# Kernel tuning notes

Hardware: AMD Instinct MI355X
Metric: run time of the kernel (lower is better)

Reference implementation:

```python
import jax, jax.numpy as jnp
import numpy as np

N, E, C, L = 50000, 800000, 64, 3  # nodes, edges, channels, message-passing layers
EPS = 1e-5  # torch.nn.LayerNorm default eps


def _mlp(h, W0, b0, W1, b1, W2, b2, g, beta):
    # MLP(input, hidden=[C, C], output=C) with ReLU between linears, LayerNorm at end
    h = jax.nn.relu(h @ W0 + b0)
    h = jax.nn.relu(h @ W1 + b1)
    h = h @ W2 + b2
    mu = jnp.mean(h, axis=-1, keepdims=True)
    var = jnp.var(h, axis=-1, keepdims=True)
    return (h - mu) * jax.lax.rsqrt(var + EPS) * g + beta


def setup_inputs() -> dict:
    key = jax.random.key(0)
    ks = jax.random.split(key, 12)
    def w(k, shape, fan_in):
        return (jax.random.normal(k, shape, jnp.float32) / np.float32(np.sqrt(fan_in)))
    return {
        "x": jax.random.normal(ks[0], (N, C), jnp.float32),
        "e": jax.random.normal(ks[1], (E, C), jnp.float32),
        "edge_index": jax.random.randint(ks[2], (2, E), 0, N),
        # edge_updater MLP params, stacked over L layers
        "ew0": w(ks[3], (L, 3 * C, C), 3 * C), "eb0": jnp.zeros((L, C), jnp.float32),
        "ew1": w(ks[4], (L, C, C), C),         "eb1": jnp.zeros((L, C), jnp.float32),
        "ew2": w(ks[5], (L, C, C), C),         "eb2": jnp.zeros((L, C), jnp.float32),
        "eg": jnp.ones((L, C), jnp.float32),   "ebt": jnp.zeros((L, C), jnp.float32),
        # node_updater MLP params
        "nw0": w(ks[6], (L, 2 * C, C), 2 * C), "nb0": jnp.zeros((L, C), jnp.float32),
        "nw1": w(ks[7], (L, C, C), C),         "nb1": jnp.zeros((L, C), jnp.float32),
        "nw2": w(ks[8], (L, C, C), C),         "nb2": jnp.zeros((L, C), jnp.float32),
        "ng": jnp.ones((L, C), jnp.float32),   "nbt": jnp.zeros((L, C), jnp.float32),
    }


def reference(x, e, edge_index, ew0, eb0, ew1, eb1, ew2, eb2, eg, ebt,
              nw0, nb0, nw1, nb1, nw2, nb2, ng, nbt):
    src, dst = edge_index[0], edge_index[1]
    for i in range(L):
        # e += edge_updater(cat(x_src, x_dst, e))
        e = e + _mlp(jnp.concatenate([x[src], x[dst], e], axis=1),
                     ew0[i], eb0[i], ew1[i], eb1[i], ew2[i], eb2[i], eg[i], ebt[i])
        # EdgeAggregation(aggr='add'): scatter-add edge features at target nodes
        agg = jax.ops.segment_sum(e, dst, num_segments=N)
        # x += node_updater(cat(x, agg))
        x = x + _mlp(jnp.concatenate([x, agg], axis=1),
                     nw0[i], nb0[i], nw1[i], nb1[i], nw2[i], nb2[i], ng[i], nbt[i])
    return (x, e)
```

## Files before the change

kernel.cpp:

```cpp
#include <hip/hip_runtime.h>

#define CH 64

using bf16x8 = __attribute__((ext_vector_type(8))) short;
using f32x4  = __attribute__((ext_vector_type(4))) float;

__device__ __forceinline__ unsigned short f2bf(float f) {
  unsigned int u = __float_as_uint(f);
  u = (u + 0x7FFFu + ((u >> 16) & 1u)) >> 16;
  return (unsigned short)u;
}

__device__ __forceinline__ bf16x8 pack8(f32x4 a, f32x4 b) {
  bf16x8 r;
  r[0] = (short)f2bf(a[0]); r[1] = (short)f2bf(a[1]);
  r[2] = (short)f2bf(a[2]); r[3] = (short)f2bf(a[3]);
  r[4] = (short)f2bf(b[0]); r[5] = (short)f2bf(b[1]);
  r[6] = (short)f2bf(b[2]); r[7] = (short)f2bf(b[3]);
  return r;
}

#define E0S 200
#define S64 72
#define N0S 136
#define Y68 68

#define EW0_L 0
#define EW1_L 12800
#define EW2_L 17408
#define EW_TOT 22016
#define E_LDS 39424

#define NW0_L 0
#define NW1_L 8704
#define NW2_L 13312
#define NW_TOT 17920
#define N_LDS 26624

#define WS_NW 66048
#define WS_AGG_B    262144
#define WS_ROWPTR_B 13062144
#define WS_NEXT_B   13262208
#define WS_EID_B    13462208

__global__ void prep_w(const float* __restrict__ ew0, const float* __restrict__ ew1,
                       const float* __restrict__ ew2, const float* __restrict__ nw0,
                       const float* __restrict__ nw1, const float* __restrict__ nw2,
                       unsigned short* __restrict__ ws) {
  int i = blockIdx.x * 256 + threadIdx.x;
  if (i < 36864) {
    int l = i / 12288, r = i % 12288, k = r / 64, n = r % 64;
    ws[l * EW_TOT + EW0_L + n * E0S + k] = f2bf(ew0[i]);
  } else if (i < 49152) {
    int j = i - 36864, l = j / 4096, r = j % 4096, k = r / 64, n = r % 64;
    ws[l * EW_TOT + EW1_L + n * S64 + k] = f2bf(ew1[j]);
  } else if (i < 61440) {
    int j = i - 49152, l = j / 4096, r = j % 4096, k = r / 64, n = r % 64;
    ws[l * EW_TOT + EW2_L + n * S64 + k] = f2bf(ew2[j]);
  } else if (i < 86016) {
    int j = i - 61440, l = j / 8192, r = j % 8192, k = r / 64, n = r % 64;
    ws[WS_NW + l * NW_TOT + NW0_L + n * N0S + k] = f2bf(nw0[j]);
  } else if (i < 98304) {
    int j = i - 86016, l = j / 4096, r = j % 4096, k = r / 64, n = r % 64;
    ws[WS_NW + l * NW_TOT + NW1_L + n * S64 + k] = f2bf(nw1[j]);
  } else if (i < 110592) {
    int j = i - 98304, l = j / 4096, r = j % 4096, k = r / 64, n = r % 64;
    ws[WS_NW + l * NW_TOT + NW2_L + n * S64 + k] = f2bf(nw2[j]);
  }
}

__global__ void hist_k(const int* __restrict__ dst, int* __restrict__ counts, int nE) {
  int i = blockIdx.x * 256 + threadIdx.x;
  if (i < nE) atomicAdd(counts + dst[i], 1);
}

__global__ void scan_k(const int* __restrict__ counts, int* __restrict__ row_ptr,
                       int* __restrict__ next, int n) {
  __shared__ int wsum[16];
  __shared__ int chunk_tot;
  __shared__ int base_sh;
  const int tid = threadIdx.x, lane = tid & 63, wv = tid >> 6;
  if (tid == 0) { base_sh = 0; row_ptr[0] = 0; }
  __syncthreads();
  for (int start = 0; start < n; start += 4096) {
    int idx = start + tid * 4;
    int v[4], s = 0;
#pragma unroll
    for (int k = 0; k < 4; ++k) { v[k] = (idx + k < n) ? counts[idx + k] : 0; s += v[k]; }
    int incl = s;
#pragma unroll
    for (int off = 1; off < 64; off <<= 1) {
      int t = __shfl_up(incl, off, 64);
      if (lane >= off) incl += t;
    }
    if (lane == 63) wsum[wv] = incl;
    __syncthreads();
    if (wv == 0 && lane < 16) {
      int w = wsum[lane];
      int wincl = w;
#pragma unroll
      for (int off = 1; off < 16; off <<= 1) {
        int t = __shfl_up(wincl, off, 16);
        if (lane >= off) wincl += t;
      }
      if (lane == 15) chunk_tot = wincl;
      wsum[lane] = wincl - w;
    }
    __syncthreads();
    int run = base_sh + wsum[wv] + (incl - s);
#pragma unroll
    for (int k = 0; k < 4; ++k) {
      int i = idx + k;
      if (i < n) { next[i] = run; run += v[k]; row_ptr[i + 1] = run; }
    }
    __syncthreads();
    if (tid == 0) base_sh += chunk_tot;
    __syncthreads();
  }
}

__global__ void scatter_k(const int* __restrict__ dst, int* __restrict__ next,
                          int* __restrict__ eid, int nE) {
  int i = blockIdx.x * 256 + threadIdx.x;
  if (i < nE) {
    int p = atomicAdd(next + dst[i], 1);
    eid[p] = i;
  }
}

__global__ __launch_bounds__(512, 4)
void edge_kernel(const float* __restrict__ x, const float* e_in, float* e_out,
                 const int* __restrict__ src, const int* __restrict__ dst,
                 const unsigned short* __restrict__ wg,
                 const float* __restrict__ b0, const float* __restrict__ b1,
                 const float* __restrict__ b2, const float* __restrict__ gam,
                 const float* __restrict__ bet, int nE) {
  __shared__ unsigned short lds[E_LDS];
  const int tid = threadIdx.x;
  {
    const uint4* s4 = (const uint4*)wg;
    uint4* d4 = (uint4*)lds;
    for (int i = tid; i < EW_TOT / 8; i += 512) d4[i] = s4[i];
  }
  __syncthreads();

  const int wave = tid >> 6, lane = tid & 63;
  const int quad = lane >> 4, l15 = lane & 15;
  const int EHo = EW_TOT + wave * 2176;
  float* yb = (float*)(lds + EHo);

  float b0c[4], b1c[4], b2c[4], gc[4], btc[4];
#pragma unroll
  for (int j = 0; j < 4; ++j) {
    int col = j * 16 + l15;
    b0c[j] = b0[col]; b1c[j] = b1[col]; b2c[j] = b2[col];
    gc[j] = gam[col]; btc[j] = bet[col];
  }

  const int o1 = quad * 8, o2 = 32 + quad * 8;
  const int gstride = gridDim.x * 128;

  int row0 = blockIdx.x * 128 + wave * 16 + l15;
  int si = src[row0], di = dst[row0];

  for (int base = blockIdx.x * 128; base < nE; base += gstride) {
    const int row = base + wave * 16 + l15;
    const float* er = e_in + (size_t)row * CH;
    f32x4 ve0 = *(const f32x4*)(er + o1);
    f32x4 ve1 = *(const f32x4*)(er + o1 + 4);
    f32x4 ve2 = *(const f32x4*)(er + o2);
    f32x4 ve3 = *(const f32x4*)(er + o2 + 4);
    const float* xs = x + (size_t)si * CH;
    const float* xd = x + (size_t)di * CH;
    bf16x8 af[6];
    {
      f32x4 a0 = *(const f32x4*)(xs + o1);
      f32x4 a1 = *(const f32x4*)(xs + o1 + 4);
      f32x4 a2 = *(const f32x4*)(xs + o2);
      f32x4 a3 = *(const f32x4*)(xs + o2 + 4);
      af[0] = pack8(a0, a1); af[1] = pack8(a2, a3);
    }
    {
      f32x4 a0 = *(const f32x4*)(xd + o1);
      f32x4 a1 = *(const f32x4*)(xd + o1 + 4);
      f32x4 a2 = *(const f32x4*)(xd + o2);
      f32x4 a3 = *(const f32x4*)(xd + o2 + 4);
      af[2] = pack8(a0, a1); af[3] = pack8(a2, a3);
    }
    af[4] = pack8(ve0, ve1); af[5] = pack8(ve2, ve3);

    {
      int nbase = base + gstride;
      if (nbase < nE) {
        int nrow = nbase + wave * 16 + l15;
        si = src[nrow]; di = dst[nrow];
      }
    }

    f32x4 acc0[4];
#pragma unroll
    for (int j = 0; j < 4; ++j) acc0[j] = (f32x4){0.f, 0.f, 0.f, 0.f};
#pragma unroll
    for (int t = 0; t < 6; ++t) {
#pragma unroll
      for (int j = 0; j < 4; ++j) {
        bf16x8 b = *(const bf16x8*)(lds + EW0_L + (j * 16 + l15) * E0S + t * 32 + quad * 8);
        acc0[j] = __builtin_amdgcn_mfma_f32_16x16x32_bf16(af[t], b, acc0[j], 0, 0, 0);
      }
    }
#pragma unroll
    for (int j = 0; j < 4; ++j) {
      int col = j * 16 + l15;
#pragma unroll
      for (int r = 0; r < 4; ++r) {
        float v = fmaxf(acc0[j][r] + b0c[j], 0.f);
        lds[EHo + (quad * 4 + r) * S64 + col] = f2bf(v);
      }
    }
    f32x4 acc1[4];
#pragma unroll
    for (int j = 0; j < 4; ++j) acc1[j] = (f32x4){0.f, 0.f, 0.f, 0.f};
#pragma unroll
    for (int t = 0; t < 2; ++t) {
      bf16x8 a = *(const bf16x8*)(lds + EHo + l15 * S64 + t * 32 + quad * 8);
#pragma unroll
      for (int j = 0; j < 4; ++j) {
        bf16x8 b = *(const bf16x8*)(lds + EW1_L + (j * 16 + l15) * S64 + t * 32 + quad * 8);
        acc1[j] = __builtin_amdgcn_mfma_f32_16x16x32_bf16(a, b, acc1[j], 0, 0, 0);
      }
    }
#pragma unroll
    for (int j = 0; j < 4; ++j) {
      int col = j * 16 + l15;
#pragma unroll
      for (int r = 0; r < 4; ++r) {
        float v = fmaxf(acc1[j][r] + b1c[j], 0.f);
        lds[EHo + (quad * 4 + r) * S64 + col] = f2bf(v);
      }
    }
    f32x4 acc2[4];
#pragma unroll
    for (int j = 0; j < 4; ++j) acc2[j] = (f32x4){0.f, 0.f, 0.f, 0.f};
#pragma unroll
    for (int t = 0; t < 2; ++t) {
      bf16x8 a = *(const bf16x8*)(lds + EHo + l15 * S64 + t * 32 + quad * 8);
#pragma unroll
      for (int j = 0; j < 4; ++j) {
        bf16x8 b = *(const bf16x8*)(lds + EW2_L + (j * 16 + l15) * S64 + t * 32 + quad * 8);
        acc2[j] = __builtin_amdgcn_mfma_f32_16x16x32_bf16(a, b, acc2[j], 0, 0, 0);
      }
    }
    float vv[4][4], s1[4], s2[4];
#pragma unroll
    for (int r = 0; r < 4; ++r) { s1[r] = 0.f; s2[r] = 0.f; }
#pragma unroll
    for (int j = 0; j < 4; ++j)
#pragma unroll
      for (int r = 0; r < 4; ++r) {
        float v = acc2[j][r] + b2c[j];
        vv[j][r] = v; s1[r] += v; s2[r] += v * v;
      }
#pragma unroll
    for (int m = 1; m < 16; m <<= 1)
#pragma unroll
      for (int r = 0; r < 4; ++r) {
        s1[r] += __shfl_xor(s1[r], m, 64);
        s2[r] += __shfl_xor(s2[r], m, 64);
      }
#pragma unroll
    for (int r = 0; r < 4; ++r) {
      float mean = s1[r] * 0.015625f;
      float var = s2[r] * 0.015625f - mean * mean;
      float rstd = rsqrtf(var + 1e-5f);
#pragma unroll
      for (int j = 0; j < 4; ++j) {
        float y = (vv[j][r] - mean) * rstd * gc[j] + btc[j];
        yb[(quad * 4 + r) * Y68 + j * 16 + l15] = y;
      }
    }
    f32x4 y0 = *(const f32x4*)(yb + l15 * Y68 + o1);
    f32x4 y1 = *(const f32x4*)(yb + l15 * Y68 + o1 + 4);
    f32x4 y2 = *(const f32x4*)(yb + l15 * Y68 + o2);
    f32x4 y3 = *(const f32x4*)(yb + l15 * Y68 + o2 + 4);
    float* eo = e_out + (size_t)row * CH;
    *(f32x4*)(eo + o1)     = ve0 + y0;
    *(f32x4*)(eo + o1 + 4) = ve1 + y1;
    *(f32x4*)(eo + o2)     = ve2 + y2;
    *(f32x4*)(eo + o2 + 4) = ve3 + y3;
  }
}

__global__ __launch_bounds__(256)
void agg_kernel(const float* __restrict__ e, const int* __restrict__ row_ptr,
                const int* __restrict__ eid, float* __restrict__ agg, int nN) {
  int node = blockIdx.x * 4 + (threadIdx.x >> 6);
  if (node >= nN) return;
  int lane = threadIdx.x & 63;
  int quad = lane >> 4, l15 = lane & 15;
  int r0 = row_ptr[node], r1 = row_ptr[node + 1];
  f32x4 s = (f32x4){0.f, 0.f, 0.f, 0.f};
  f32x4 s2 = (f32x4){0.f, 0.f, 0.f, 0.f};
  int i = r0 + quad;
  for (; i + 4 < r1; i += 8) {
    int e0 = eid[i], e1 = eid[i + 4];
    f32x4 a = *(const f32x4*)(e + (size_t)e0 * CH + l15 * 4);
    f32x4 b = *(const f32x4*)(e + (size_t)e1 * CH + l15 * 4);
    s += a; s2 += b;
  }
  for (; i < r1; i += 4) {
    int e0 = eid[i];
    s += *(const f32x4*)(e + (size_t)e0 * CH + l15 * 4);
  }
  s += s2;
#pragma unroll
  for (int c = 0; c < 4; ++c) {
    s[c] += __shfl_xor(s[c], 16, 64);
    s[c] += __shfl_xor(s[c], 32, 64);
  }
  if (quad == 0) *(f32x4*)(agg + (size_t)node * CH + l15 * 4) = s;
}

__global__ __launch_bounds__(256, 3)
void node_kernel(const float* x_in, const float* __restrict__ agg_in,
                 const unsigned short* __restrict__ wg,
                 const float* __restrict__ b0, const float* __restrict__ b1,
                 const float* __restrict__ b2, const float* __restrict__ gam,
                 const float* __restrict__ bet, float* x_out, int nN) {
  __shared__ unsigned short lds[N_LDS];
  const int tid = threadIdx.x;
  {
    const uint4* s4 = (const uint4*)wg;
    uint4* d4 = (uint4*)lds;
    for (int i = tid; i < NW_TOT / 8; i += 256) d4[i] = s4[i];
  }
  __syncthreads();

  const int wave = tid >> 6, lane = tid & 63;
  const int quad = lane >> 4, l15 = lane & 15;
  const int NHo = NW_TOT + wave * 2176;
  float* yb = (float*)(lds + NHo);

  float b0c[4], b1c[4], b2c[4], gc[4], btc[4];
#pragma unroll
  for (int j = 0; j < 4; ++j) {
    int col = j * 16 + l15;
    b0c[j] = b0[col]; b1c[j] = b1[col]; b2c[j] = b2[col];
    gc[j] = gam[col]; btc[j] = bet[col];
  }

  const int o1 = quad * 8, o2 = 32 + quad * 8;

  for (int base = blockIdx.x * 64; base < nN; base += gridDim.x * 64) {
    const int nbase = base + wave * 16;
    if (nbase >= nN) continue;
    const int row = nbase + l15;
    const float* xr = x_in + (size_t)row * CH;
    const float* ar = agg_in + (size_t)row * CH;
    f32x4 vx0 = *(const f32x4*)(xr + o1);
    f32x4 vx1 = *(const f32x4*)(xr + o1 + 4);
    f32x4 vx2 = *(const f32x4*)(xr + o2);
    f32x4 vx3 = *(const f32x4*)(xr + o2 + 4);
    bf16x8 af[4];
    af[0] = pack8(vx0, vx1); af[1] = pack8(vx2, vx3);
    {
      f32x4 a0 = *(const f32x4*)(ar + o1);
      f32x4 a1 = *(const f32x4*)(ar + o1 + 4);
      f32x4 a2 = *(const f32x4*)(ar + o2);
      f32x4 a3 = *(const f32x4*)(ar + o2 + 4);
      af[2] = pack8(a0, a1); af[3] = pack8(a2, a3);
    }

    f32x4 acc0[4];
#pragma unroll
    for (int j = 0; j < 4; ++j) acc0[j] = (f32x4){0.f, 0.f, 0.f, 0.f};
#pragma unroll
    for (int t = 0; t < 4; ++t) {
#pragma unroll
      for (int j = 0; j < 4; ++j) {
        bf16x8 b = *(const bf16x8*)(lds + NW0_L + (j * 16 + l15) * N0S + t * 32 + quad * 8);
        acc0[j] = __builtin_amdgcn_mfma_f32_16x16x32_bf16(af[t], b, acc0[j], 0, 0, 0);
      }
    }
#pragma unroll
    for (int j = 0; j < 4; ++j) {
      int col = j * 16 + l15;
#pragma unroll
      for (int r = 0; r < 4; ++r) {
        float v = fmaxf(acc0[j][r] + b0c[j], 0.f);
        lds[NHo + (quad * 4 + r) * S64 + col] = f2bf(v);
      }
    }
    f32x4 acc1[4];
#pragma unroll
    for (int j = 0; j < 4; ++j) acc1[j] = (f32x4){0.f, 0.f, 0.f, 0.f};
#pragma unroll
    for (int t = 0; t < 2; ++t) {
      bf16x8 a = *(const bf16x8*)(lds + NHo + l15 * S64 + t * 32 + quad * 8);
#pragma unroll
      for (int j = 0; j < 4; ++j) {
        bf16x8 b = *(const bf16x8*)(lds + NW1_L + (j * 16 + l15) * S64 + t * 32 + quad * 8);
        acc1[j] = __builtin_amdgcn_mfma_f32_16x16x32_bf16(a, b, acc1[j], 0, 0, 0);
      }
    }
#pragma unroll
    for (int j = 0; j < 4; ++j) {
      int col = j * 16 + l15;
#pragma unroll
      for (int r = 0; r < 4; ++r) {
        float v = fmaxf(acc1[j][r] + b1c[j], 0.f);
        lds[NHo + (quad * 4 + r) * S64 + col] = f2bf(v);
      }
    }
    f32x4 acc2[4];
#pragma unroll
    for (int j = 0; j < 4; ++j) acc2[j] = (f32x4){0.f, 0.f, 0.f, 0.f};
#pragma unroll
    for (int t = 0; t < 2; ++t) {
      bf16x8 a = *(const bf16x8*)(lds + NHo + l15 * S64 + t * 32 + quad * 8);
#pragma unroll
      for (int j = 0; j < 4; ++j) {
        bf16x8 b = *(const bf16x8*)(lds + NW2_L + (j * 16 + l15) * S64 + t * 32 + quad * 8);
        acc2[j] = __builtin_amdgcn_mfma_f32_16x16x32_bf16(a, b, acc2[j], 0, 0, 0);
      }
    }
    float vv[4][4], s1[4], s2[4];
#pragma unroll
    for (int r = 0; r < 4; ++r) { s1[r] = 0.f; s2[r] = 0.f; }
#pragma unroll
    for (int j = 0; j < 4; ++j)
#pragma unroll
      for (int r = 0; r < 4; ++r) {
        float v = acc2[j][r] + b2c[j];
        vv[j][r] = v; s1[r] += v; s2[r] += v * v;
      }
#pragma unroll
    for (int m = 1; m < 16; m <<= 1)
#pragma unroll
      for (int r = 0; r < 4; ++r) {
        s1[r] += __shfl_xor(s1[r], m, 64);
        s2[r] += __shfl_xor(s2[r], m, 64);
      }
#pragma unroll
    for (int r = 0; r < 4; ++r) {
      float mean = s1[r] * 0.015625f;
      float var = s2[r] * 0.015625f - mean * mean;
      float rstd = rsqrtf(var + 1e-5f);
#pragma unroll
      for (int j = 0; j < 4; ++j) {
        float y = (vv[j][r] - mean) * rstd * gc[j] + btc[j];
        yb[(quad * 4 + r) * Y68 + j * 16 + l15] = y;
      }
    }
    f32x4 y0 = *(const f32x4*)(yb + l15 * Y68 + o1);
    f32x4 y1 = *(const f32x4*)(yb + l15 * Y68 + o1 + 4);
    f32x4 y2 = *(const f32x4*)(yb + l15 * Y68 + o2);
    f32x4 y3 = *(const f32x4*)(yb + l15 * Y68 + o2 + 4);
    float* xo = x_out + (size_t)row * CH;
    *(f32x4*)(xo + o1)     = vx0 + y0;
    *(f32x4*)(xo + o1 + 4) = vx1 + y1;
    *(f32x4*)(xo + o2)     = vx2 + y2;
    *(f32x4*)(xo + o2 + 4) = vx3 + y3;
  }
}

extern "C" void kernel_launch(void* const* d_in, const int* in_sizes, int n_in,
                              void* d_out, int out_size, void* d_ws, size_t ws_size,
                              hipStream_t stream) {
  const float* x0 = (const float*)d_in[0];
  const float* e0 = (const float*)d_in[1];
  const int* ei  = (const int*)d_in[2];
  const float* ew0 = (const float*)d_in[3];
  const float* eb0 = (const float*)d_in[4];
  const float* ew1 = (const float*)d_in[5];
  const float* eb1 = (const float*)d_in[6];
  const float* ew2 = (const float*)d_in[7];
  const float* eb2 = (const float*)d_in[8];
  const float* eg  = (const float*)d_in[9];
  const float* ebt = (const float*)d_in[10];
  const float* nw0 = (const float*)d_in[11];
  const float* nb0 = (const float*)d_in[12];
  const float* nw1 = (const float*)d_in[13];
  const float* nb1 = (const float*)d_in[14];
  const float* nw2 = (const float*)d_in[15];
  const float* nb2 = (const float*)d_in[16];
  const float* ng  = (const float*)d_in[17];
  const float* nbt = (const float*)d_in[18];

  const int N = in_sizes[0] / CH;
  const int E = in_sizes[1] / CH;
  const int* src = ei;
  const int* dst = ei + E;

  float* xout = (float*)d_out;
  float* eout = (float*)d_out + (size_t)N * CH;

  unsigned short* wsu = (unsigned short*)d_ws;
  float* agg    = (float*)((char*)d_ws + WS_AGG_B);
  int* row_ptr  = (int*)((char*)d_ws + WS_ROWPTR_B);
  int* nxt      = (int*)((char*)d_ws + WS_NEXT_B);
  int* eid      = (int*)((char*)d_ws + WS_EID_B);

  prep_w<<<432, 256, 0, stream>>>(ew0, ew1, ew2, nw0, nw1, nw2, wsu);

  hipMemsetAsync(nxt, 0, (size_t)N * sizeof(int), stream);
  hist_k<<<(E + 255) / 256, 256, 0, stream>>>(dst, nxt, E);
  scan_k<<<1, 1024, 0, stream>>>(nxt, row_ptr, nxt, N);
  scatter_k<<<(E + 255) / 256, 256, 0, stream>>>(dst, nxt, eid, E);

  for (int l = 0; l < 3; ++l) {
    const float* xin = (l == 0) ? x0 : xout;
    const float* einp = (l == 0) ? e0 : eout;
    edge_kernel<<<512, 512, 0, stream>>>(
        xin, einp, eout, src, dst, wsu + l * EW_TOT,
        eb0 + l * CH, eb1 + l * CH, eb2 + l * CH, eg + l * CH, ebt + l * CH, E);
    agg_kernel<<<(N + 3) / 4, 256, 0, stream>>>(eout, row_ptr, eid, agg, N);
    node_kernel<<<782, 256, 0, stream>>>(
        xin, agg, wsu + WS_NW + l * NW_TOT,
        nb0 + l * CH, nb1 + l * CH, nb2 + l * CH, ng + l * CH, nbt + l * CH,
        xout, N);
  }
}
```

Baseline: 969.9 us.

## Fuse edge scatter-add into edge kernel via dst-sorted processing and segmented atomics

```diff
diff --git a/kernel.cpp b/kernel.cpp
--- a/kernel.cpp
+++ b/kernel.cpp
@@ -42,6 +42,8 @@
 #define WS_ROWPTR_B 13062144
 #define WS_NEXT_B   13262208
 #define WS_EID_B    13462208
+#define WS_SRCS_B   16662208
+#define WS_DSTS_B   19862208
 
 __global__ void prep_w(const float* __restrict__ ew0, const float* __restrict__ ew1,
                        const float* __restrict__ ew2, const float* __restrict__ nw0,
@@ -119,18 +121,24 @@
   }
 }
 
-__global__ void scatter_k(const int* __restrict__ dst, int* __restrict__ next,
-                          int* __restrict__ eid, int nE) {
+__global__ void scatter_k(const int* __restrict__ src, const int* __restrict__ dst,
+                          int* __restrict__ next, int* __restrict__ eid,
+                          int* __restrict__ srcs, int* __restrict__ dsts, int nE) {
   int i = blockIdx.x * 256 + threadIdx.x;
   if (i < nE) {
-    int p = atomicAdd(next + dst[i], 1);
+    int d = dst[i];
+    int p = atomicAdd(next + d, 1);
     eid[p] = i;
+    srcs[p] = src[i];
+    dsts[p] = d;
   }
 }
 
 __global__ __launch_bounds__(512, 4)
-void edge_kernel(const float* __restrict__ x, const float* e_in, float* e_out,
-                 const int* __restrict__ src, const int* __restrict__ dst,
+void edge_kernel(const float* __restrict__ x, const float* __restrict__ e_in,
+                 float* __restrict__ e_out, float* __restrict__ agg,
+                 const int* __restrict__ eid, const int* __restrict__ srcs,
+                 const int* __restrict__ dsts,
                  const unsigned short* __restrict__ wg,
                  const float* __restrict__ b0, const float* __restrict__ b1,
                  const float* __restrict__ b2, const float* __restrict__ gam,
@@ -160,18 +168,18 @@
   const int o1 = quad * 8, o2 = 32 + quad * 8;
   const int gstride = gridDim.x * 128;
 
-  int row0 = blockIdx.x * 128 + wave * 16 + l15;
-  int si = src[row0], di = dst[row0];
+  int p0 = blockIdx.x * 128 + wave * 16 + l15;
+  int ei = eid[p0], si = srcs[p0], di = dsts[p0];
 
   for (int base = blockIdx.x * 128; base < nE; base += gstride) {
-    const int row = base + wave * 16 + l15;
-    const float* er = e_in + (size_t)row * CH;
+    const int cei = ei, csi = si, d = di;
+    const float* er = e_in + (size_t)cei * CH;
     f32x4 ve0 = *(const f32x4*)(er + o1);
     f32x4 ve1 = *(const f32x4*)(er + o1 + 4);
     f32x4 ve2 = *(const f32x4*)(er + o2);
     f32x4 ve3 = *(const f32x4*)(er + o2 + 4);
-    const float* xs = x + (size_t)si * CH;
-    const float* xd = x + (size_t)di * CH;
+    const float* xs = x + (size_t)csi * CH;
+    const float* xd = x + (size_t)d * CH;
     bf16x8 af[6];
     {
       f32x4 a0 = *(const f32x4*)(xs + o1);
@@ -192,8 +200,8 @@
     {
       int nbase = base + gstride;
       if (nbase < nE) {
-        int nrow = nbase + wave * 16 + l15;
-        si = src[nrow]; di = dst[nrow];
+        int np = nbase + wave * 16 + l15;
+        ei = eid[np]; si = srcs[np]; di = dsts[np];
       }
     }
 
@@ -278,46 +286,41 @@
         yb[(quad * 4 + r) * Y68 + j * 16 + l15] = y;
       }
     }
-    f32x4 y0 = *(const f32x4*)(yb + l15 * Y68 + o1);
-    f32x4 y1 = *(const f32x4*)(yb + l15 * Y68 + o1 + 4);
-    f32x4 y2 = *(const f32x4*)(yb + l15 * Y68 + o2);
-    f32x4 y3 = *(const f32x4*)(yb + l15 * Y68 + o2 + 4);
-    float* eo = e_out + (size_t)row * CH;
-    *(f32x4*)(eo + o1)     = ve0 + y0;
-    *(f32x4*)(eo + o1 + 4) = ve1 + y1;
-    *(f32x4*)(eo + o2)     = ve2 + y2;
-    *(f32x4*)(eo + o2 + 4) = ve3 + y3;
-  }
-}
-
-__global__ __launch_bounds__(256)
-void agg_kernel(const float* __restrict__ e, const int* __restrict__ row_ptr,
-                const int* __restrict__ eid, float* __restrict__ agg, int nN) {
-  int node = blockIdx.x * 4 + (threadIdx.x >> 6);
-  if (node >= nN) return;
-  int lane = threadIdx.x & 63;
-  int quad = lane >> 4, l15 = lane & 15;
-  int r0 = row_ptr[node], r1 = row_ptr[node + 1];
-  f32x4 s = (f32x4){0.f, 0.f, 0.f, 0.f};
-  f32x4 s2 = (f32x4){0.f, 0.f, 0.f, 0.f};
-  int i = r0 + quad;
-  for (; i + 4 < r1; i += 8) {
-    int e0 = eid[i], e1 = eid[i + 4];
-    f32x4 a = *(const f32x4*)(e + (size_t)e0 * CH + l15 * 4);
-    f32x4 b = *(const f32x4*)(e + (size_t)e1 * CH + l15 * 4);
-    s += a; s2 += b;
-  }
-  for (; i < r1; i += 4) {
-    int e0 = eid[i];
-    s += *(const f32x4*)(e + (size_t)e0 * CH + l15 * 4);
-  }
-  s += s2;
-#pragma unroll
-  for (int c = 0; c < 4; ++c) {
-    s[c] += __shfl_xor(s[c], 16, 64);
-    s[c] += __shfl_xor(s[c], 32, 64);
-  }
-  if (quad == 0) *(f32x4*)(agg + (size_t)node * CH + l15 * 4) = s;
+    f32x4 w0 = ve0 + *(const f32x4*)(yb + l15 * Y68 + o1);
+    f32x4 w1 = ve1 + *(const f32x4*)(yb + l15 * Y68 + o1 + 4);
+    f32x4 w2 = ve2 + *(const f32x4*)(yb + l15 * Y68 + o2);
+    f32x4 w3 = ve3 + *(const f32x4*)(yb + l15 * Y68 + o2 + 4);
+    float* eo = e_out + (size_t)cei * CH;
+    *(f32x4*)(eo + o1)     = w0;
+    *(f32x4*)(eo + o1 + 4) = w1;
+    *(f32x4*)(eo + o2)     = w2;
+    *(f32x4*)(eo + o2 + 4) = w3;
+
+#pragma unroll
+    for (int off = 1; off < 16; off <<= 1) {
+      int dp = __shfl_up(d, off, 16);
+      f32x4 t0, t1, t2, t3;
+#pragma unroll
+      for (int c = 0; c < 4; ++c) {
+        t0[c] = __shfl_up(w0[c], off, 16);
+        t1[c] = __shfl_up(w1[c], off, 16);
+        t2[c] = __shfl_up(w2[c], off, 16);
+        t3[c] = __shfl_up(w3[c], off, 16);
+      }
+      if (l15 >= off && dp == d) { w0 += t0; w1 += t1; w2 += t2; w3 += t3; }
+    }
+    int dn = __shfl_down(d, 1, 16);
+    if (l15 == 15 || dn != d) {
+      float* ag = agg + (size_t)d * CH;
+#pragma unroll
+      for (int c = 0; c < 4; ++c) {
+        atomicAdd(ag + o1 + c,     w0[c]);
+        atomicAdd(ag + o1 + 4 + c, w1[c]);
+        atomicAdd(ag + o2 + c,     w2[c]);
+        atomicAdd(ag + o2 + 4 + c, w3[c]);
+      }
+    }
+  }
 }
 
 __global__ __launch_bounds__(256, 3)
@@ -499,21 +502,23 @@
   int* row_ptr  = (int*)((char*)d_ws + WS_ROWPTR_B);
   int* nxt      = (int*)((char*)d_ws + WS_NEXT_B);
   int* eid      = (int*)((char*)d_ws + WS_EID_B);
+  int* srcs     = (int*)((char*)d_ws + WS_SRCS_B);
+  int* dsts     = (int*)((char*)d_ws + WS_DSTS_B);
 
   prep_w<<<432, 256, 0, stream>>>(ew0, ew1, ew2, nw0, nw1, nw2, wsu);
 
   hipMemsetAsync(nxt, 0, (size_t)N * sizeof(int), stream);
   hist_k<<<(E + 255) / 256, 256, 0, stream>>>(dst, nxt, E);
   scan_k<<<1, 1024, 0, stream>>>(nxt, row_ptr, nxt, N);
-  scatter_k<<<(E + 255) / 256, 256, 0, stream>>>(dst, nxt, eid, E);
+  scatter_k<<<(E + 255) / 256, 256, 0, stream>>>(src, dst, nxt, eid, srcs, dsts, E);
 
   for (int l = 0; l < 3; ++l) {
     const float* xin = (l == 0) ? x0 : xout;
     const float* einp = (l == 0) ? e0 : eout;
+    hipMemsetAsync(agg, 0, (size_t)N * CH * sizeof(float), stream);
     edge_kernel<<<512, 512, 0, stream>>>(
-        xin, einp, eout, src, dst, wsu + l * EW_TOT,
+        xin, einp, eout, agg, eid, srcs, dsts, wsu + l * EW_TOT,
         eb0 + l * CH, eb1 + l * CH, eb2 + l * CH, eg + l * CH, ebt + l * CH, E);
-    agg_kernel<<<(N + 3) / 4, 256, 0, stream>>>(eout, row_ptr, eid, agg, N);
     node_kernel<<<782, 256, 0, stream>>>(
         xin, agg, wsu + WS_NW + l * NW_TOT,
         nb0 + l * CH, nb1 + l * CH, nb2 + l * CH, ng + l * CH, nbt + l * CH,
```

Measured after the change: 1.226 ms. 26.4% more time.
